# Kernel optimization log

Measured on AMD Instinct MI355X. Metric: run time of the kernel, lower is better.

## Reference

```python
import jax, jax.numpy as jnp
import numpy as np

INPUT_SIZE = 1024
HIDDEN = 1024
NUM_LAYERS = 2
BATCH = 64
SEQ = 512


def setup_inputs() -> dict:
    key = jax.random.key(0)
    ks = jax.random.split(key, 5)
    k = 1.0 / np.sqrt(HIDDEN)  # torch nn.Linear default init bound
    x = jax.random.normal(ks[0], (BATCH, SEQ, INPUT_SIZE), dtype=jnp.float32)
    # stacked per-layer weights (input_size == hidden_size so shapes are uniform)
    W_ih = jax.random.uniform(ks[1], (NUM_LAYERS, 4 * HIDDEN, INPUT_SIZE), minval=-k, maxval=k, dtype=jnp.float32)
    b_ih = jax.random.uniform(ks[2], (NUM_LAYERS, 4 * HIDDEN), minval=-k, maxval=k, dtype=jnp.float32)
    W_hh = jax.random.uniform(ks[3], (NUM_LAYERS, 4 * HIDDEN, HIDDEN), minval=-k, maxval=k, dtype=jnp.float32)
    b_hh = jax.random.uniform(ks[4], (NUM_LAYERS, 4 * HIDDEN), minval=-k, maxval=k, dtype=jnp.float32)
    return {"x": x, "W_ih": W_ih, "b_ih": b_ih, "W_hh": W_hh, "b_hh": b_hh}


def _lstm_forward(x, W_ih, b_ih, W_hh, b_hh):
    B = x.shape[0]
    H = W_hh.shape[-1]
    L = W_ih.shape[0]
    h0 = jnp.zeros((L, B, H), dtype=x.dtype)
    c0 = jnp.zeros((L, B, H), dtype=x.dtype)

    def step(carry, x_t):
        h, c = carry  # each [L, B, H]
        inp = x_t  # [B, I]
        new_h, new_c = [], []
        for l in range(L):
            gates = inp @ W_ih[l].T + b_ih[l] + h[l] @ W_hh[l].T + b_hh[l]  # [B, 4H]
            i_g, f_g, g_g, o_g = jnp.split(gates, 4, axis=1)
            i_g = jax.nn.sigmoid(i_g)
            f_g = jax.nn.sigmoid(f_g)
            g_g = jnp.tanh(g_g)
            o_g = jax.nn.sigmoid(o_g)
            cy = f_g * c[l] + i_g * g_g
            hy = o_g * jnp.tanh(cy)
            new_h.append(hy)
            new_c.append(cy)
            inp = hy
        return (jnp.stack(new_h), jnp.stack(new_c)), inp

    (h_f, c_f), outs = jax.lax.scan(step, (h0, c0), jnp.swapaxes(x, 0, 1))
    outputs = jnp.swapaxes(outs, 0, 1)  # [B, S, H]
    return outputs, h_f[-1], c_f[-1]


def reference(x, W_ih, b_ih, W_hh, b_hh):
    outputs, h_last, c_last = _lstm_forward(x, W_ih, b_ih, W_hh, b_hh)
    return outputs, (h_last, c_last)
```

## Files before the change

### kernel.cpp

```cpp
#include <hip/hip_runtime.h>
#include <hip/hip_bf16.h>

#define SEQ 512
#define HD 1024
#define NWG 256
#define TPB 512
#define RED_OFF 131072
#define LDS_BYTES (131072 + 32768)
#define OUT_H 33554432ull
#define OUT_C 33619968ull
#define RMASK 31
#define HSLOT 131072

typedef __bf16 bf16x8 __attribute__((ext_vector_type(8)));
typedef float f32x4 __attribute__((ext_vector_type(4)));

__device__ __forceinline__ unsigned short f2bf(float f) {
  __hip_bfloat16 b = __float2bfloat16(f);
  return __builtin_bit_cast(unsigned short, b);
}
__device__ __forceinline__ float bf2f(unsigned short s) {
  return __builtin_bit_cast(float, (unsigned)s << 16);
}

__device__ __forceinline__ float sigm(float v) { return 1.f / (1.f + __expf(-v)); }
__device__ __forceinline__ float tanh_(float v) {
  float av = fabsf(v);
  float e = __expf(-2.f * av);
  float t = (1.f - e) / (1.f + e);
  return copysignf(t, v);
}

__device__ __forceinline__ void gl2lds(const void* g, void* l) {
  __builtin_amdgcn_global_load_lds(
      (const __attribute__((address_space(1))) void*)g,
      (__attribute__((address_space(3))) void*)l, 16, 0, 0);
}

__device__ __forceinline__ void wave_wait_ge(const unsigned* a, unsigned v) {
  while (__hip_atomic_load(a, __ATOMIC_RELAXED, __HIP_MEMORY_SCOPE_AGENT) < v)
    __builtin_amdgcn_s_sleep(1);
  __builtin_amdgcn_wave_barrier();
  asm volatile("" ::: "memory");
}

__global__ __launch_bounds__(TPB, 2) void lstm_main(
    const float* __restrict__ x,
    const float* __restrict__ Wih_f,
    const float* __restrict__ Whh_f,
    const float* __restrict__ bias,
    unsigned short* h0p, unsigned short* h1p,
    float* __restrict__ out,
    unsigned* bar) {
  __shared__ char smem[LDS_BYTES];
  float* red = (float*)(smem + RED_OFF);

  unsigned* go0 = bar + 8192;
  unsigned* go1 = bar + 8192 + 32;

  const int w = blockIdx.x;
  const int tid = threadIdx.x;
  const int layer = w >> 7;
  const int tl = w & 127;
  const int j0 = tl << 3;
  const int lane = tid & 63;
  const int kw = tid >> 6;
  const int cl = lane & 15;
  const int rg = lane >> 4;
  const int kbase = kw << 8;
  const bool isx = (layer == 0) && (kw < 4);

  uint4 whi[16], wlo[16];
#pragma unroll
  for (int i = 0; i < 16; ++i) {
    const int nt = i & 1, ks = i >> 1;
    const int c = nt * 16 + cl;
    const int grow = ((c >> 3) << 10) + j0 + (c & 7);
    const int kglob = kbase + (ks << 5) + (rg << 3);
    const float* src = (kglob < HD)
        ? (Wih_f + (((size_t)layer << 22) + ((size_t)grow << 10) + kglob))
        : (Whh_f + (((size_t)layer << 22) + ((size_t)grow << 10) + (kglob - HD)));
    union { unsigned short s2[8]; uint4 v; } uh, ul;
#pragma unroll
    for (int e = 0; e < 8; ++e) {
      const float vv = src[e];
      const unsigned short hb = f2bf(vv);
      uh.s2[e] = hb;
      ul.s2[e] = f2bf(vv - bf2f(hb));
    }
    whi[i] = uh.v;
    wlo[i] = ul.v;
  }

  const int u_ = cl & 7;
  const float bi  = bias[(layer << 12) + j0 + u_];
  const float bf_ = bias[(layer << 12) + 1024 + j0 + u_];
  const float bg  = bias[(layer << 12) + 2048 + j0 + u_];
  const float bo  = bias[(layer << 12) + 3072 + j0 + u_];

  float creg[4];
#pragma unroll
  for (int i = 0; i < 4; ++i) creg[i] = 0.f;

  char* sbase = smem + (kw << 14);
  const int srow = lane >> 3;
  const int sslot = (lane & 7) ^ srow;
  const int hkc = (kw & 3) << 3;

  __syncthreads();

  for (int t = 0; t < SEQ; ++t) {
    const unsigned e = (unsigned)(t + 1);

    if (layer == 0) {
      if (kw >= 4) wave_wait_ge(go0, (unsigned)t);
    } else {
      if (kw < 4) wave_wait_ge(go0, e);
      else        wave_wait_ge(go1, (unsigned)t);
    }

    f32x4 acc[4][2];
#pragma unroll
    for (int mt = 0; mt < 4; ++mt) {
      acc[mt][0] = (f32x4){0.f, 0.f, 0.f, 0.f};
      acc[mt][1] = (f32x4){0.f, 0.f, 0.f, 0.f};
    }

    if (isx) {
      const float* xb = x + ((size_t)(srow * SEQ + t) << 10) + kbase + (sslot << 2);
#pragma unroll
      for (int i = 0; i < 8; ++i)
        gl2lds(xb + (size_t)i * 4194304, sbase + (i << 10));
#pragma unroll
      for (int s = 0; s < 8; ++s) {
        char* cb = sbase + ((s & 1) << 13);
        if (s < 7) {
          char* nb = sbase + (((s + 1) & 1) << 13);
#pragma unroll
          for (int i = 0; i < 8; ++i)
            gl2lds(xb + (size_t)i * 4194304 + ((s + 1) << 5), nb + (i << 10));
          asm volatile("s_waitcnt vmcnt(8)" ::: "memory");
        } else {
          asm volatile("s_waitcnt vmcnt(0)" ::: "memory");
        }
        const bf16x8 bh0 = __builtin_bit_cast(bf16x8, whi[(s << 1)]);
        const bf16x8 bh1 = __builtin_bit_cast(bf16x8, whi[(s << 1) + 1]);
        const bf16x8 bl0 = __builtin_bit_cast(bf16x8, wlo[(s << 1)]);
        const bf16x8 bl1 = __builtin_bit_cast(bf16x8, wlo[(s << 1) + 1]);
#pragma unroll
        for (int mt = 0; mt < 4; ++mt) {
          const int row = (mt << 4) + cl;
          const int wv = row & 7;
          const char* rb = cb + ((row >> 3) << 10) + (wv << 7);
          const float4 f0 = *(const float4*)(rb + (((rg << 1) ^ wv) << 4));
          const float4 f1 = *(const float4*)(rb + ((((rg << 1) | 1) ^ wv) << 4));
          union { unsigned short s2[8]; uint4 v; } uh, ul;
          const float ee[8] = {f0.x, f0.y, f0.z, f0.w, f1.x, f1.y, f1.z, f1.w};
#pragma unroll
          for (int e2 = 0; e2 < 8; ++e2) {
            const unsigned uu = __builtin_bit_cast(unsigned, ee[e2]);
            uh.s2[e2] = (unsigned short)(uu >> 16);
            ul.s2[e2] = f2bf(ee[e2] - __builtin_bit_cast(float, uu & 0xffff0000u));
          }
          const bf16x8 ah = __builtin_bit_cast(bf16x8, uh.v);
          const bf16x8 al = __builtin_bit_cast(bf16x8, ul.v);
          acc[mt][0] = __builtin_amdgcn_mfma_f32_16x16x32_bf16(ah, bh0, acc[mt][0], 0, 0, 0);
          acc[mt][1] = __builtin_amdgcn_mfma_f32_16x16x32_bf16(ah, bh1, acc[mt][1], 0, 0, 0);
          acc[mt][0] = __builtin_amdgcn_mfma_f32_16x16x32_bf16(al, bh0, acc[mt][0], 0, 0, 0);
          acc[mt][1] = __builtin_amdgcn_mfma_f32_16x16x32_bf16(al, bh1, acc[mt][1], 0, 0, 0);
          acc[mt][0] = __builtin_amdgcn_mfma_f32_16x16x32_bf16(ah, bl0, acc[mt][0], 0, 0, 0);
          acc[mt][1] = __builtin_amdgcn_mfma_f32_16x16x32_bf16(ah, bl1, acc[mt][1], 0, 0, 0);
        }
      }
    } else {
      const unsigned short* hsl;
      if (layer == 0)  hsl = h0p + (size_t)((t - 1) & RMASK) * HSLOT;
      else if (kw < 4) hsl = h0p + (size_t)(t & RMASK) * HSLOT;
      else             hsl = h1p + (size_t)((t - 1) & RMASK) * HSLOT;
      const unsigned short* hb = hsl + (srow << 11) + (hkc << 6) + (sslot << 3);
#pragma unroll
      for (int i = 0; i < 8; ++i)
        gl2lds(hb + (i << 14), sbase + (i << 10));
#pragma unroll
      for (int s = 0; s < 8; ++s) {
        char* cb = sbase + ((s & 1) << 13);
        if (s < 7) {
          char* nb = sbase + (((s + 1) & 1) << 13);
#pragma unroll
          for (int i = 0; i < 8; ++i)
            gl2lds(hb + (i << 14) + ((s + 1) << 6), nb + (i << 10));
          asm volatile("s_waitcnt vmcnt(8)" ::: "memory");
        } else {
          asm volatile("s_waitcnt vmcnt(0)" ::: "memory");
        }
        const bf16x8 bh0 = __builtin_bit_cast(bf16x8, whi[(s << 1)]);
        const bf16x8 bh1 = __builtin_bit_cast(bf16x8, whi[(s << 1) + 1]);
        const bf16x8 bl0 = __builtin_bit_cast(bf16x8, wlo[(s << 1)]);
        const bf16x8 bl1 = __builtin_bit_cast(bf16x8, wlo[(s << 1) + 1]);
#pragma unroll
        for (int mt = 0; mt < 4; ++mt) {
          const int row = (mt << 4) + cl;
          const int wv = row & 7;
          const char* rb = cb + ((row >> 3) << 10) + (wv << 7);
          const bf16x8 ah = __builtin_bit_cast(bf16x8, *(const uint4*)(rb + ((rg ^ wv) << 4)));
          const bf16x8 al = __builtin_bit_cast(bf16x8, *(const uint4*)(rb + (((4 | rg) ^ wv) << 4)));
          acc[mt][0] = __builtin_amdgcn_mfma_f32_16x16x32_bf16(ah, bh0, acc[mt][0], 0, 0, 0);
          acc[mt][1] = __builtin_amdgcn_mfma_f32_16x16x32_bf16(ah, bh1, acc[mt][1], 0, 0, 0);
          acc[mt][0] = __builtin_amdgcn_mfma_f32_16x16x32_bf16(al, bh0, acc[mt][0], 0, 0, 0);
          acc[mt][1] = __builtin_amdgcn_mfma_f32_16x16x32_bf16(al, bh1, acc[mt][1], 0, 0, 0);
          acc[mt][0] = __builtin_amdgcn_mfma_f32_16x16x32_bf16(ah, bl0, acc[mt][0], 0, 0, 0);
          acc[mt][1] = __builtin_amdgcn_mfma_f32_16x16x32_bf16(ah, bl1, acc[mt][1], 0, 0, 0);
        }
      }
    }

    if (kw >= 4) {
      float* rp = red + ((kw - 4) << 11) + lane;
#pragma unroll
      for (int mt = 0; mt < 4; ++mt)
#pragma unroll
        for (int nt = 0; nt < 2; ++nt)
#pragma unroll
          for (int r = 0; r < 4; ++r)
            rp[((mt << 3) + (nt << 2) + r) << 6] = acc[mt][nt][r];
    }
    __syncthreads();
    if (kw < 4) {
      float* rp = red + (kw << 11) + lane;
#pragma unroll
      for (int mt = 0; mt < 4; ++mt)
#pragma unroll
        for (int nt = 0; nt < 2; ++nt)
#pragma unroll
          for (int r = 0; r < 4; ++r) {
            const int idx = ((mt << 3) + (nt << 2) + r) << 6;
            acc[mt][nt][r] += rp[idx];
            rp[idx] = acc[mt][nt][r];
          }
    }
    __syncthreads();

    float hsv[4] = {0.f, 0.f, 0.f, 0.f}, csv[4] = {0.f, 0.f, 0.f, 0.f};
    if (kw < 4) {
      float g0[4], g1[4];
#pragma unroll
      for (int r = 0; r < 4; ++r) {
        const int i0x = (((kw << 3) + r) << 6) + lane;
        const int i1x = (((kw << 3) + 4 + r) << 6) + lane;
        g0[r] = red[i0x] + red[2048 + i0x] + red[4096 + i0x] + red[6144 + i0x];
        g1[r] = red[i1x] + red[2048 + i1x] + red[4096 + i1x] + red[6144 + i1x];
      }
      if (layer == 0 && t >= 32) wave_wait_ge(go1, (unsigned)(t - 31));
      const int wsl = t & RMASK;
      unsigned short* hd = (layer ? h1p : h0p) + (size_t)wsl * HSLOT;
      const int ch = tl >> 2;
      const int cpos = ((tl & 3) << 3) + u_;
#pragma unroll
      for (int r = 0; r < 4; ++r) {
        const float a0 = g0[r], a1 = g1[r];
        const float a0x = __shfl_xor(a0, 8);
        const float a1x = __shfl_xor(a1, 8);
        const bool lo = (cl < 8);
        const float vi = (lo ? a0 : a0x) + bi;
        const float vf = (lo ? a0x : a0) + bf_;
        const float vg = (lo ? a1 : a1x) + bg;
        const float vo = (lo ? a1x : a1) + bo;
        const float ig = sigm(vi), fg = sigm(vf), gg = tanh_(vg), og = sigm(vo);
        const float cn = fg * creg[r] + ig * gg;
        creg[r] = cn;
        const float h = og * tanh_(cn);
        hsv[r] = h; csv[r] = cn;
        if (lo) {
          const int b = (kw << 4) + (rg << 2) + r;
          const size_t hx = ((size_t)b << 11) + (ch << 6) + cpos;
          const unsigned short hb16 = f2bf(h);
          const unsigned short lb16 = f2bf(h - bf2f(hb16));
          __hip_atomic_store(hd + hx, hb16, __ATOMIC_RELAXED, __HIP_MEMORY_SCOPE_AGENT);
          __hip_atomic_store(hd + hx + 32, lb16, __ATOMIC_RELAXED, __HIP_MEMORY_SCOPE_AGENT);
        }
      }
      asm volatile("s_waitcnt vmcnt(0)" ::: "memory");
    }
    __syncthreads();

    if (tid == 0)
      __hip_atomic_store(bar + (w << 5), e, __ATOMIC_RELAXED, __HIP_MEMORY_SCOPE_AGENT);

    if (layer && kw < 4 && cl < 8) {
#pragma unroll
      for (int r = 0; r < 4; ++r) {
        const int b = (kw << 4) + (rg << 2) + r;
        out[((size_t)b * SEQ + t) * HD + j0 + u_] = hsv[r];
        if (t == SEQ - 1) {
          out[OUT_H + (size_t)(b << 10) + j0 + u_] = hsv[r];
          out[OUT_C + (size_t)(b << 10) + j0 + u_] = csv[r];
        }
      }
    }

    if (tl == 0) {
      __syncthreads();
      if (tid >= 1 && tid < 128) {
        const unsigned* pf = bar + (((layer << 7) + tid) << 5);
        while (__hip_atomic_load(pf, __ATOMIC_RELAXED, __HIP_MEMORY_SCOPE_AGENT) < e)
          __builtin_amdgcn_s_sleep(1);
      }
      __syncthreads();
      if (tid == 0)
        __hip_atomic_store(layer ? go1 : go0, e, __ATOMIC_RELAXED, __HIP_MEMORY_SCOPE_AGENT);
    }

    if ((t & 15) == 15) __builtin_amdgcn_fence(__ATOMIC_ACQUIRE, "agent");
  }
}

__global__ void lstm_prep(const float* __restrict__ bih, const float* __restrict__ bhh,
                          float* __restrict__ bias,
                          unsigned short* __restrict__ h0p, unsigned short* __restrict__ h1p,
                          unsigned* __restrict__ bar) {
  const size_t i0 = (size_t)blockIdx.x * blockDim.x + threadIdx.x;
  const size_t stride = (size_t)gridDim.x * blockDim.x;
  for (size_t idx = i0; idx < 8192; idx += stride) bias[idx] = bih[idx] + bhh[idx];
  const ushort4 z = make_ushort4(0, 0, 0, 0);
  const size_t so = ((size_t)RMASK * HSLOT) >> 2;
  for (size_t idx = i0; idx < 32768; idx += stride) {
    ((ushort4*)h0p)[so + idx] = z;
    ((ushort4*)h1p)[so + idx] = z;
  }
  for (size_t idx = i0; idx < 8256; idx += stride) bar[idx] = 0u;
}

extern "C" void kernel_launch(void* const* d_in, const int* in_sizes, int n_in,
                              void* d_out, int out_size, void* d_ws, size_t ws_size,
                              hipStream_t stream) {
  const float* x     = (const float*)d_in[0];
  const float* Wih_f = (const float*)d_in[1];
  const float* bih   = (const float*)d_in[2];
  const float* Whh_f = (const float*)d_in[3];
  const float* bhh   = (const float*)d_in[4];
  float* out = (float*)d_out;

  char* ws = (char*)d_ws;
  float* bias           = (float*)(ws);
  unsigned* bar         = (unsigned*)(ws + 65536);
  unsigned short* h0p   = (unsigned short*)(ws + (1ull << 20));
  unsigned short* h1p   = (unsigned short*)(ws + (1ull << 20) + (8ull << 20));

  hipLaunchKernelGGL(lstm_prep, dim3(256), dim3(256), 0, stream,
                     bih, bhh, bias, h0p, h1p, bar);

  hipLaunchKernelGGL(lstm_main, dim3(NWG), dim3(TPB), 0, stream,
                     x, Wih_f, Whh_f, bias, h0p, h1p, out, bar);
}
```

Before: 6.419 ms.

## Replace leader-gathered flags with per-step atomic arrival counters

Replaces the two-level barrier, where workgroup 0 of each layer polled 127 per-block flags and then published a go flag, with 64 rotating per-step counters per layer. Each block increments the counter with an atomic add and waiters poll until it reaches 128 times the epoch. This takes a full flag-gather and republish hop off the critical path of each serial timestep. The cost is contended atomics on a single cache line per step. The barrier area needs to be zeroed correctly, which depends on the prep code that is not shown.

```diff
diff --git a/kernel.cpp b/kernel.cpp
--- a/kernel.cpp
+++ b/kernel.cpp
@@ -37,8 +37,10 @@
       (__attribute__((address_space(3))) void*)l, 16, 0, 0);
 }
 
-__device__ __forceinline__ void wave_wait_ge(const unsigned* a, unsigned v) {
-  while (__hip_atomic_load(a, __ATOMIC_RELAXED, __HIP_MEMORY_SCOPE_AGENT) < v)
+__device__ __forceinline__ void wait_step(const unsigned* cbase, int T) {
+  const unsigned* p = cbase + ((unsigned)(T & 63) << 5);
+  const unsigned tgt = 128u * (unsigned)((T >> 6) + 1);
+  while (__hip_atomic_load(p, __ATOMIC_RELAXED, __HIP_MEMORY_SCOPE_AGENT) < tgt)
     __builtin_amdgcn_s_sleep(1);
   __builtin_amdgcn_wave_barrier();
   asm volatile("" ::: "memory");
@@ -55,8 +57,8 @@
   __shared__ char smem[LDS_BYTES];
   float* red = (float*)(smem + RED_OFF);
 
-  unsigned* go0 = bar + 8192;
-  unsigned* go1 = bar + 8192 + 32;
+  unsigned* c0 = bar;
+  unsigned* c1 = bar + 2048;
 
   const int w = blockIdx.x;
   const int tid = threadIdx.x;
@@ -110,13 +112,11 @@
   __syncthreads();
 
   for (int t = 0; t < SEQ; ++t) {
-    const unsigned e = (unsigned)(t + 1);
-
     if (layer == 0) {
-      if (kw >= 4) wave_wait_ge(go0, (unsigned)t);
+      if (kw >= 4 && t >= 1) wait_step(c0, t - 1);
     } else {
-      if (kw < 4) wave_wait_ge(go0, e);
-      else        wave_wait_ge(go1, (unsigned)t);
+      if (kw < 4) wait_step(c0, t);
+      else if (t >= 1) wait_step(c1, t - 1);
     }
 
     f32x4 acc[4][2];
@@ -250,7 +250,7 @@
         g0[r] = red[i0x] + red[2048 + i0x] + red[4096 + i0x] + red[6144 + i0x];
         g1[r] = red[i1x] + red[2048 + i1x] + red[4096 + i1x] + red[6144 + i1x];
       }
-      if (layer == 0 && t >= 32) wave_wait_ge(go1, (unsigned)(t - 31));
+      if (layer == 0 && t >= 32) wait_step(c1, t - 32);
       const int wsl = t & RMASK;
       unsigned short* hd = (layer ? h1p : h0p) + (size_t)wsl * HSLOT;
       const int ch = tl >> 2;
@@ -283,8 +283,10 @@
     }
     __syncthreads();
 
-    if (tid == 0)
-      __hip_atomic_store(bar + (w << 5), e, __ATOMIC_RELAXED, __HIP_MEMORY_SCOPE_AGENT);
+    if (tid == 0) {
+      unsigned* slot = (layer ? c1 : c0) + ((unsigned)(t & 63) << 5);
+      (void)__hip_atomic_fetch_add(slot, 1u, __ATOMIC_RELAXED, __HIP_MEMORY_SCOPE_AGENT);
+    }
 
     if (layer && kw < 4 && cl < 8) {
 #pragma unroll
@@ -296,18 +298,6 @@
           out[OUT_C + (size_t)(b << 10) + j0 + u_] = csv[r];
         }
       }
-    }
-
-    if (tl == 0) {
-      __syncthreads();
-      if (tid >= 1 && tid < 128) {
-        const unsigned* pf = bar + (((layer << 7) + tid) << 5);
-        while (__hip_atomic_load(pf, __ATOMIC_RELAXED, __HIP_MEMORY_SCOPE_AGENT) < e)
-          __builtin_amdgcn_s_sleep(1);
-      }
-      __syncthreads();
-      if (tid == 0)
-        __hip_atomic_store(layer ? go1 : go0, e, __ATOMIC_RELAXED, __HIP_MEMORY_SCOPE_AGENT);
     }
 
     if ((t & 15) == 15) __builtin_amdgcn_fence(__ATOMIC_ACQUIRE, "agent");
```

After: 7.569 ms. 17.9% more time.
